# Optimization experiments

Hardware: AMD Instinct MI355X
Metric: run time of the kernel (lower is better)

## Reference

```python
import jax, jax.numpy as jnp
import numpy as np
import math

B, L, D, H, DFF = 8, 2048, 512, 8, 2048
FACTOR = 5

def setup_inputs() -> dict:
    key = jax.random.key(0)
    ks = jax.random.split(key, 20)
    r = lambda k, shape, s=0.02: (jax.random.normal(k, shape, jnp.float32) * s)
    return {
        'encoder_output': jax.random.normal(ks[0], (B, L, D), jnp.float32),
        'Wq': r(ks[1], (D, D)), 'bq': jnp.zeros((D,), jnp.float32),
        'Wk': r(ks[2], (D, D)), 'bk': jnp.zeros((D,), jnp.float32),
        'Wv': r(ks[3], (D, D)), 'bv': jnp.zeros((D,), jnp.float32),
        'Wo': r(ks[4], (D, D)), 'bo': jnp.zeros((D,), jnp.float32),
        'W1': r(ks[5], (DFF, D)), 'b1': jnp.zeros((DFF,), jnp.float32),
        'W2': r(ks[6], (D, DFF)), 'b2': jnp.zeros((D,), jnp.float32),
        'g1': jnp.ones((D,), jnp.float32), 'be1': jnp.zeros((D,), jnp.float32),
        'g2': jnp.ones((D,), jnp.float32), 'be2': jnp.zeros((D,), jnp.float32),
        'Wout': r(ks[7], (D, 1)), 'bout': jnp.zeros((1,), jnp.float32),
    }

def _layernorm(x, g, b, eps=1e-5):
    m = x.mean(-1, keepdims=True)
    v = x.var(-1, keepdims=True)
    return (x - m) / jnp.sqrt(v + eps) * g + b

def reference(encoder_output, Wq, bq, Wk, bk, Wv, bv, Wo, bo,
              W1, b1, W2, b2, g1, be1, g2, be2, Wout, bout):
    x = encoder_output  # [B, L, D]
    dh = D // H
    u = min(L, FACTOR * math.ceil(math.log(L)))  # number of active queries (static)

    # multi-head projections -> [B, H, L, dh]
    q = (x @ Wq + bq).reshape(B, L, H, dh).transpose(0, 2, 1, 3)
    k = (x @ Wk + bk).reshape(B, L, H, dh).transpose(0, 2, 1, 3)
    v = (x @ Wv + bv).reshape(B, L, H, dh).transpose(0, 2, 1, 3)

    # deterministic prob-sparse: sparsity measurement over all keys
    scores = jnp.einsum('bhld,bhsd->bhls', q, k) / math.sqrt(dh)  # [B,H,L,L]
    M = scores.max(-1) - scores.mean(-1)                           # [B,H,L]
    top_idx = jax.lax.top_k(M, u)[1]                               # [B,H,u]

    top_scores = jnp.take_along_axis(scores, top_idx[..., None], axis=2)  # [B,H,u,L]
    attn = jax.nn.softmax(top_scores, axis=-1)
    top_out = jnp.einsum('bhus,bhsd->bhud', attn, v)               # [B,H,u,dh]

    # lazy queries get mean(V); active queries get true attention
    ctx = jnp.broadcast_to(v.mean(axis=2, keepdims=True), (B, H, L, dh))
    bi = jnp.arange(B)[:, None, None]
    hi = jnp.arange(H)[None, :, None]
    ctx = ctx.at[bi, hi, top_idx].set(top_out)                     # [B,H,L,dh]

    attn_out = ctx.transpose(0, 2, 1, 3).reshape(B, L, D) @ Wo + bo  # [B,L,D]

    # decoder body: mean-pool, residual norms, pointwise conv FFN (eval-mode dropout = identity)
    a = attn_out.mean(axis=1)                 # [B, D]
    a = _layernorm(a + a, g1, be1)[:, None, :]  # [B, 1, D]  (a + dropout(a))

    ff = jax.nn.relu(a @ W1.T + b1)           # conv1d k=1 == linear, [B,1,DFF]
    ff = ff @ W2.T + b2                       # [B,1,D]
    out = _layernorm(a + ff, g2, be2)         # [B,1,D]

    forecasts = (out @ Wout + bout).squeeze(-1)  # [B,1]
    return forecasts, out
```

## Files before the change

### kernel.cpp

```cpp
#include <hip/hip_runtime.h>
#include <hip/hip_bf16.h>


#define B_   8
#define L_   2048
#define D_   512
#define H_   8
#define DH_  64
#define DFF_ 2048
#define U_   40
#define BH_  64
#define NM_  16384
#define NCK_ 16
#define CKS_ 128

typedef __bf16 bf16_t;
typedef __bf16 bf16x8 __attribute__((ext_vector_type(8)));
typedef float  f32x4  __attribute__((ext_vector_type(4)));

__device__ __forceinline__ void gl_lds16(const bf16_t* g, bf16_t* l) {
    __builtin_amdgcn_global_load_lds(
        (const __attribute__((address_space(1))) unsigned int*)g,
        (__attribute__((address_space(3))) unsigned int*)l, 16, 0, 0);
}

__global__ void k_cvt(const float* __restrict__ X, bf16_t* __restrict__ Xb) {
    size_t g = (size_t)blockIdx.x * 256 + threadIdx.x;
    const float4* xp = (const float4*)&X[g * 8];
    float4 f0 = xp[0], f1 = xp[1];
    bf16x8 hv;
    hv[0]=(bf16_t)f0.x; hv[1]=(bf16_t)f0.y; hv[2]=(bf16_t)f0.z; hv[3]=(bf16_t)f0.w;
    hv[4]=(bf16_t)f1.x; hv[5]=(bf16_t)f1.y; hv[6]=(bf16_t)f1.z; hv[7]=(bf16_t)f1.w;
    *(bf16x8*)&Xb[g * 8] = hv;
}

__global__ void k_transpose_w(const float* __restrict__ Wq, const float* __restrict__ Wk,
                              const float* __restrict__ Wv, bf16_t* __restrict__ WT) {
    __shared__ float tile[64][65];
    int blk = blockIdx.x;
    int mat = blk >> 6, tl = blk & 63;
    int tr = (tl >> 3) << 6;
    int tc = (tl & 7) << 6;
    const float* W = (mat == 0) ? Wq : (mat == 1) ? Wk : Wv;
    int t = threadIdx.x;
    #pragma unroll
    for (int i = 0; i < 16; ++i) {
        int e = t + i * 256, r = e >> 6, c = e & 63;
        tile[r][c] = W[(size_t)(tr + r) * 512 + tc + c];
    }
    __syncthreads();
    #pragma unroll
    for (int i = 0; i < 16; ++i) {
        int e = t + i * 256, r = e >> 6, c = e & 63;
        WT[(size_t)(mat * 512 + tc + r) * 512 + tr + c] = (bf16_t)tile[c][r];
    }
}

__global__ __launch_bounds__(256) void k_qkv(const bf16_t* __restrict__ Xb,
        const bf16_t* __restrict__ WT,
        const float* __restrict__ bq, const float* __restrict__ bk, const float* __restrict__ bv,
        bf16_t* __restrict__ Qb, bf16_t* __restrict__ Kb, float* __restrict__ Vf) {
    __shared__ bf16_t As[128 * 64];
    __shared__ bf16_t Bs[128 * 64];
    int t = threadIdx.x;
    int m0 = blockIdx.y * 128;
    int n0 = blockIdx.x * 128;
    int wv = t >> 6, lane = t & 63, lr = lane & 15, qd = lane >> 4;
    int wm = (wv & 1) * 64, wn = (wv >> 1) * 64;
    f32x4 acc[4][4];
    #pragma unroll
    for (int a = 0; a < 4; ++a)
        #pragma unroll
        for (int b = 0; b < 4; ++b) acc[a][b] = (f32x4){0.f, 0.f, 0.f, 0.f};

    for (int kt = 0; kt < 8; ++kt) {
        bf16x8 areg[4], breg[4];
        #pragma unroll
        for (int i = 0; i < 4; ++i) {
            int ch = i * 256 + t, r = ch >> 3, cs = ch & 7;
            areg[i] = *(const bf16x8*)&Xb[(size_t)(m0 + r) * 512 + kt * 64 + cs * 8];
            breg[i] = *(const bf16x8*)&WT[(size_t)(n0 + r) * 512 + kt * 64 + cs * 8];
        }
        __syncthreads();
        #pragma unroll
        for (int i = 0; i < 4; ++i) {
            int ch = i * 256 + t, r = ch >> 3, cs = ch & 7, c = cs ^ (r & 7);
            *(bf16x8*)&As[(r * 8 + c) * 8] = areg[i];
            *(bf16x8*)&Bs[(r * 8 + c) * 8] = breg[i];
        }
        __syncthreads();
        bf16x8 af[4][2], bfg[4][2];
        #pragma unroll
        for (int rf = 0; rf < 4; ++rf) {
            int row = wm + rf * 16 + lr;
            #pragma unroll
            for (int ks = 0; ks < 2; ++ks)
                af[rf][ks] = *(bf16x8*)&As[row * 64 + (((ks * 4 + qd) ^ (row & 7)) * 8)];
        }
        #pragma unroll
        for (int cf = 0; cf < 4; ++cf) {
            int row = wn + cf * 16 + lr;
            #pragma unroll
            for (int ks = 0; ks < 2; ++ks)
                bfg[cf][ks] = *(bf16x8*)&Bs[row * 64 + (((ks * 4 + qd) ^ (row & 7)) * 8)];
        }
        #pragma unroll
        for (int cf = 0; cf < 4; ++cf)
            #pragma unroll
            for (int rf = 0; rf < 4; ++rf) {
                acc[rf][cf] = __builtin_amdgcn_mfma_f32_16x16x32_bf16(af[rf][0], bfg[cf][0], acc[rf][cf], 0, 0, 0);
                acc[rf][cf] = __builtin_amdgcn_mfma_f32_16x16x32_bf16(af[rf][1], bfg[cf][1], acc[rf][cf], 0, 0, 0);
            }
    }
    int sec = n0 >> 9;
    const float* bias = (sec == 0) ? bq : (sec == 1) ? bk : bv;
    #pragma unroll
    for (int rf = 0; rf < 4; ++rf) {
        #pragma unroll
        for (int r = 0; r < 4; ++r) {
            int m = m0 + wm + rf * 16 + qd * 4 + r;
            int b = m >> 11, l = m & 2047;
            #pragma unroll
            for (int cf = 0; cf < 4; ++cf) {
                int n = n0 + wn + cf * 16 + lr;
                int nn = n & 511;
                int h = nn >> 6, d = nn & 63;
                float val = acc[rf][cf][r] + bias[nn];
                size_t oidx = ((size_t)(b * 8 + h) * L_ + l) * 64 + d;
                if (sec == 0)      Qb[oidx] = (bf16_t)val;
                else if (sec == 1) Kb[oidx] = (bf16_t)val;
                else               Vf[oidx] = val;
            }
        }
    }
}

__global__ __launch_bounds__(256) void k_rowmax(const bf16_t* __restrict__ Qb,
        const bf16_t* __restrict__ Kb, const float* __restrict__ kpart,
        float* __restrict__ Mv) {
    __shared__ bf16_t Ks[128 * 64];
    __shared__ float ksum_s[64];
    __shared__ float dot_s[128];
    int t = threadIdx.x;
    int bh = blockIdx.y;
    int row0 = blockIdx.x * 128;
    int wv = t >> 6, lane = t & 63, lr = lane & 15, qd = lane >> 4;
    size_t base = (size_t)bh * L_ * DH_;
    if (t < 64) {
        float a = 0.f;
        #pragma unroll
        for (int seg = 0; seg < 8; ++seg) a += kpart[(bh * 8 + seg) * 64 + t];
        ksum_s[t] = a;
    }
    bf16x8 af[2][2];
    #pragma unroll
    for (int rf = 0; rf < 2; ++rf)
        #pragma unroll
        for (int ks = 0; ks < 2; ++ks)
            af[rf][ks] = *(const bf16x8*)&Qb[base + (size_t)(row0 + wv * 32 + rf * 16 + lr) * 64 + ks * 32 + qd * 8];
    __syncthreads();
    #pragma unroll
    for (int rf = 0; rf < 2; ++rf) {
        float v = 0.f;
        #pragma unroll
        for (int ks = 0; ks < 2; ++ks)
            #pragma unroll
            for (int j = 0; j < 8; ++j)
                v += (float)af[rf][ks][j] * ksum_s[ks * 32 + qd * 8 + j];
        v += __shfl_xor(v, 16);
        v += __shfl_xor(v, 32);
        if (qd == 0) dot_s[wv * 32 + rf * 16 + lr] = v;
    }
    float pmax[2][4];
    #pragma unroll
    for (int a = 0; a < 2; ++a)
        #pragma unroll
        for (int r = 0; r < 4; ++r) pmax[a][r] = -3.4e38f;

    for (int cb = 0; cb < 16; ++cb) {
        bf16x8 kreg[4];
        #pragma unroll
        for (int i = 0; i < 4; ++i) {
            int ch = i * 256 + t, r = ch >> 3, cs = ch & 7;
            kreg[i] = *(const bf16x8*)&Kb[base + (size_t)(cb * 128 + r) * 64 + cs * 8];
        }
        __syncthreads();
        #pragma unroll
        for (int i = 0; i < 4; ++i) {
            int ch = i * 256 + t, r = ch >> 3, cs = ch & 7, c = cs ^ (r & 7);
            *(bf16x8*)&Ks[(r * 8 + c) * 8] = kreg[i];
        }
        __syncthreads();
        #pragma unroll
        for (int cf = 0; cf < 8; cf += 2) {
            int keyA = cf * 16 + lr, keyB = (cf + 1) * 16 + lr;
            bf16x8 bA0 = *(bf16x8*)&Ks[keyA * 64 + ((qd ^ (keyA & 7)) * 8)];
            bf16x8 bA1 = *(bf16x8*)&Ks[keyA * 64 + (((4 + qd) ^ (keyA & 7)) * 8)];
            bf16x8 bB0 = *(bf16x8*)&Ks[keyB * 64 + ((qd ^ (keyB & 7)) * 8)];
            bf16x8 bB1 = *(bf16x8*)&Ks[keyB * 64 + (((4 + qd) ^ (keyB & 7)) * 8)];
            #pragma unroll
            for (int rf = 0; rf < 2; ++rf) {
                f32x4 z = {0.f, 0.f, 0.f, 0.f};
                f32x4 c0 = __builtin_amdgcn_mfma_f32_16x16x32_bf16(af[rf][0], bA0, z, 0, 0, 0);
                c0 = __builtin_amdgcn_mfma_f32_16x16x32_bf16(af[rf][1], bA1, c0, 0, 0, 0);
                f32x4 c1 = __builtin_amdgcn_mfma_f32_16x16x32_bf16(af[rf][0], bB0, z, 0, 0, 0);
                c1 = __builtin_amdgcn_mfma_f32_16x16x32_bf16(af[rf][1], bB1, c1, 0, 0, 0);
                #pragma unroll
                for (int r = 0; r < 4; ++r)
                    pmax[rf][r] = fmaxf(pmax[rf][r], fmaxf(c0[r], c1[r]));
            }
        }
    }
    #pragma unroll
    for (int rf = 0; rf < 2; ++rf)
        #pragma unroll
        for (int r = 0; r < 4; ++r) {
            float v = pmax[rf][r];
            v = fmaxf(v, __shfl_xor(v, 1));
            v = fmaxf(v, __shfl_xor(v, 2));
            v = fmaxf(v, __shfl_xor(v, 4));
            v = fmaxf(v, __shfl_xor(v, 8));
            if (lr == 0) {
                int row = wv * 32 + rf * 16 + qd * 4 + r;
                Mv[bh * L_ + row0 + row] = v - dot_s[row] * (1.0f / 2048.0f);
            }
        }
}

__global__ void k_sums(const bf16_t* __restrict__ Kb, const float* __restrict__ Vf,
                       float* __restrict__ kpart, float* __restrict__ vpart) {
    __shared__ float red[32][64];
    int t = threadIdx.x;
    int seg = blockIdx.x, bh = blockIdx.y;
    int d8 = t & 7, g = t >> 3;
    size_t base = (size_t)bh * L_ * DH_ + (size_t)seg * 256 * DH_;
    float s[8];
    #pragma unroll
    for (int j = 0; j < 8; ++j) s[j] = 0.f;
    #pragma unroll
    for (int ss = 0; ss < 8; ++ss) {
        bf16x8 kk = *(const bf16x8*)&Kb[base + (size_t)(g * 8 + ss) * 64 + d8 * 8];
        #pragma unroll
        for (int j = 0; j < 8; ++j) s[j] += (float)kk[j];
    }
    #pragma unroll
    for (int j = 0; j < 8; ++j) red[g][d8 * 8 + j] = s[j];
    __syncthreads();
    if (t < 64) {
        float a = 0.f;
        #pragma unroll
        for (int gg = 0; gg < 32; ++gg) a += red[gg][t];
        kpart[(bh * 8 + seg) * 64 + t] = a;
    }
    __syncthreads();
    #pragma unroll
    for (int j = 0; j < 8; ++j) s[j] = 0.f;
    #pragma unroll
    for (int ss = 0; ss < 8; ++ss) {
        const float4* vp = (const float4*)&Vf[base + (size_t)(g * 8 + ss) * 64 + d8 * 8];
        float4 v0 = vp[0], v1 = vp[1];
        s[0]+=v0.x; s[1]+=v0.y; s[2]+=v0.z; s[3]+=v0.w;
        s[4]+=v1.x; s[5]+=v1.y; s[6]+=v1.z; s[7]+=v1.w;
    }
    __syncthreads();
    #pragma unroll
    for (int j = 0; j < 8; ++j) red[g][d8 * 8 + j] = s[j];
    __syncthreads();
    if (t < 64) {
        float a = 0.f;
        #pragma unroll
        for (int gg = 0; gg < 32; ++gg) a += red[gg][t];
        vpart[(bh * 8 + seg) * 64 + t] = a;
    }
}

__global__ void k_topk(const float* __restrict__ Mv, int* __restrict__ topidx) {
    int lane = threadIdx.x;
    int bh = blockIdx.x;
    unsigned key[32];
    #pragma unroll
    for (int j = 0; j < 32; ++j) {
        unsigned b = __float_as_uint(Mv[bh * L_ + j * 64 + lane]);
        key[j] = (b & 0x80000000u) ? ~b : (b | 0x80000000u);
    }
    unsigned lo = 0u, hi = 0xFFFFFFFFu;
    while (lo < hi) {
        unsigned mid = lo + ((hi - lo) >> 1) + 1;
        int c = 0;
        #pragma unroll
        for (int j = 0; j < 32; ++j)
            c += __popcll(__ballot(key[j] >= mid));
        if (c >= U_) lo = mid; else hi = mid - 1;
    }
    unsigned K40 = lo;
    int c_gt = 0;
    #pragma unroll
    for (int j = 0; j < 32; ++j)
        c_gt += __popcll(__ballot(key[j] > K40));
    unsigned long long lmask = (1ull << lane) - 1ull;
    int base_gt = 0, base_eq = 0;
    #pragma unroll
    for (int j = 0; j < 32; ++j) {
        bool gt = key[j] > K40, eq = key[j] == K40;
        unsigned long long mg = __ballot(gt);
        unsigned long long me = __ballot(eq);
        if (gt) {
            int pos = base_gt + __popcll(mg & lmask);
            topidx[bh * U_ + pos] = j * 64 + lane;
        } else if (eq) {
            int ep = base_eq + __popcll(me & lmask);
            if (c_gt + ep < U_)
                topidx[bh * U_ + c_gt + ep] = j * 64 + lane;
        }
        base_gt += __popcll(mg);
        base_eq += __popcll(me);
    }
}

__global__ __launch_bounds__(256) void k_attn2(const bf16_t* __restrict__ Qb,
        const bf16_t* __restrict__ Kb, const float* __restrict__ Vf,
        const int* __restrict__ topidx, float* __restrict__ part) {
    __shared__ bf16_t Qs[48 * 72];
    __shared__ bf16_t Ks[128 * 64];
    __shared__ bf16_t Vt[64 * 136];
    __shared__ float  wred[4][48];
    __shared__ float  frow[48];
    __shared__ int    tid_s[40];
    bf16_t* Ps = Ks;

    int t = threadIdx.x;
    int ck = blockIdx.x, bh = blockIdx.y;
    int c0 = ck * CKS_;
    size_t base = (size_t)bh * L_ * DH_;
    if (t < 40) tid_s[t] = topidx[bh * U_ + t];
    __syncthreads();
    #pragma unroll
    for (int i = 0; i < 4; ++i) {
        int s = i * 256 + t, r = s >> 3, cs = s & 7, c = cs ^ (r & 7);
        gl_lds16(&Kb[base + (size_t)(c0 + r) * 64 + c * 8], &Ks[s * 8]);
    }
    for (int e = t; e < 48 * 8; e += 256) {
        int r = e >> 3, c8 = e & 7;
        bf16x8 v;
        #pragma unroll
        for (int j = 0; j < 8; ++j) v[j] = (bf16_t)0.f;
        if (r < 40) v = *(const bf16x8*)&Qb[base + (size_t)tid_s[r] * 64 + c8 * 8];
        *(bf16x8*)&Qs[r * 72 + c8 * 8] = v;
    }
    #pragma unroll
    for (int i = 0; i < 8; ++i) {
        int e = t + i * 256;
        int key = e >> 4, d4 = e & 15;
        float4 v = *(const float4*)&Vf[base + (size_t)(c0 + key) * 64 + d4 * 4];
        Vt[(d4 * 4 + 0) * 136 + key] = (bf16_t)v.x;
        Vt[(d4 * 4 + 1) * 136 + key] = (bf16_t)v.y;
        Vt[(d4 * 4 + 2) * 136 + key] = (bf16_t)v.z;
        Vt[(d4 * 4 + 3) * 136 + key] = (bf16_t)v.w;
    }
    __syncthreads();

    int wv = t >> 6, lane = t & 63, lr = lane & 15, qd = lane >> 4;
    bf16x8 aq[3][2];
    #pragma unroll
    for (int tm = 0; tm < 3; ++tm)
        #pragma unroll
        for (int ks = 0; ks < 2; ++ks)
            aq[tm][ks] = *(bf16x8*)&Qs[(tm * 16 + lr) * 72 + ks * 32 + qd * 8];
    f32x4 S[3][2];
    #pragma unroll
    for (int nt = 0; nt < 2; ++nt) {
        int key = wv * 32 + nt * 16 + lr;
        bf16x8 bk0 = *(bf16x8*)&Ks[key * 64 + ((qd ^ (key & 7)) * 8)];
        bf16x8 bk1 = *(bf16x8*)&Ks[key * 64 + (((4 + qd) ^ (key & 7)) * 8)];
        #pragma unroll
        for (int tm = 0; tm < 3; ++tm) {
            f32x4 z = {0.f, 0.f, 0.f, 0.f};
            z = __builtin_amdgcn_mfma_f32_16x16x32_bf16(aq[tm][0], bk0, z, 0, 0, 0);
            S[tm][nt] = __builtin_amdgcn_mfma_f32_16x16x32_bf16(aq[tm][1], bk1, z, 0, 0, 0);
        }
    }
    float rm[3][4];
    #pragma unroll
    for (int tm = 0; tm < 3; ++tm)
        #pragma unroll
        for (int r = 0; r < 4; ++r) {
            float v = fmaxf(S[tm][0][r], S[tm][1][r]);
            v = fmaxf(v, __shfl_xor(v, 1));
            v = fmaxf(v, __shfl_xor(v, 2));
            v = fmaxf(v, __shfl_xor(v, 4));
            v = fmaxf(v, __shfl_xor(v, 8));
            rm[tm][r] = v;
        }
    if (lr == 0) {
        #pragma unroll
        for (int tm = 0; tm < 3; ++tm)
            #pragma unroll
            for (int r = 0; r < 4; ++r)
                wred[wv][tm * 16 + qd * 4 + r] = rm[tm][r];
    }
    __syncthreads();
    if (t < 48)
        frow[t] = fmaxf(fmaxf(wred[0][t], wred[1][t]), fmaxf(wred[2][t], wred[3][t]));
    __syncthreads();
    float rs_[3][4];
    #pragma unroll
    for (int tm = 0; tm < 3; ++tm) {
        #pragma unroll
        for (int r = 0; r < 4; ++r) {
            float fm = frow[tm * 16 + qd * 4 + r];
            float s0 = __expf((S[tm][0][r] - fm) * 0.125f);
            float s1 = __expf((S[tm][1][r] - fm) * 0.125f);
            Ps[(tm * 16 + qd * 4 + r) * 136 + wv * 32 + lr]      = (bf16_t)s0;
            Ps[(tm * 16 + qd * 4 + r) * 136 + wv * 32 + 16 + lr] = (bf16_t)s1;
            rs_[tm][r] = s0 + s1;
        }
    }
    #pragma unroll
    for (int tm = 0; tm < 3; ++tm)
        #pragma unroll
        for (int r = 0; r < 4; ++r) {
            float v = rs_[tm][r];
            v += __shfl_xor(v, 1);
            v += __shfl_xor(v, 2);
            v += __shfl_xor(v, 4);
            v += __shfl_xor(v, 8);
            rs_[tm][r] = v;
        }
    if (lr == 0) {
        #pragma unroll
        for (int tm = 0; tm < 3; ++tm)
            #pragma unroll
            for (int r = 0; r < 4; ++r)
                wred[wv][tm * 16 + qd * 4 + r] = rs_[tm][r];
    }
    __syncthreads();
    float* pb = &part[(((size_t)bh * NCK_ + ck) * 40) * 66];
    if (t < 40) {
        pb[t * 66 + 64] = frow[t] * 0.125f;
        pb[t * 66 + 65] = wred[0][t] + wred[1][t] + wred[2][t] + wred[3][t];
    }
    f32x4 O[3];
    #pragma unroll
    for (int tm = 0; tm < 3; ++tm) O[tm] = (f32x4){0.f, 0.f, 0.f, 0.f};
    #pragma unroll
    for (int kk = 0; kk < 4; ++kk) {
        bf16x8 bv = *(bf16x8*)&Vt[(wv * 16 + lr) * 136 + kk * 32 + qd * 8];
        #pragma unroll
        for (int tm = 0; tm < 3; ++tm) {
            bf16x8 ap = *(bf16x8*)&Ps[(tm * 16 + lr) * 136 + kk * 32 + qd * 8];
            O[tm] = __builtin_amdgcn_mfma_f32_16x16x32_bf16(ap, bv, O[tm], 0, 0, 0);
        }
    }
    #pragma unroll
    for (int tm = 0; tm < 3; ++tm)
        #pragma unroll
        for (int r = 0; r < 4; ++r) {
            int row = tm * 16 + qd * 4 + r;
            if (row < 40) pb[row * 66 + wv * 16 + lr] = O[tm][r];
        }
}

__global__ void k_attnred(const float* __restrict__ part, float* __restrict__ tout) {
    int t = threadIdx.x, bh = blockIdx.x;
    int d = t & 63, rg = t >> 6;
    const float* pb0 = &part[((size_t)bh * NCK_) * 40 * 66];
    for (int ri = 0; ri < 10; ++ri) {
        int r = rg + 4 * ri;
        float M = -3.4e38f;
        #pragma unroll
        for (int c = 0; c < NCK_; ++c) M = fmaxf(M, pb0[(c * 40 + r) * 66 + 64]);
        float lsum = 0.f, osum = 0.f;
        #pragma unroll
        for (int c = 0; c < NCK_; ++c) {
            float w = __expf(pb0[(c * 40 + r) * 66 + 64] - M);
            lsum += w * pb0[(c * 40 + r) * 66 + 65];
            osum += w * pb0[(c * 40 + r) * 66 + d];
        }
        tout[((size_t)bh * U_ + r) * 64 + d] = osum / lsum;
    }
}

__global__ void k_ctx(const float* __restrict__ vpart, const float* __restrict__ topout,
                      const float* __restrict__ Wo, const float* __restrict__ bo,
                      const float* __restrict__ g1, const float* __restrict__ be1,
                      float* __restrict__ a2) {
    __shared__ float cm[512];
    __shared__ float rs[256], rq[256];
    int t = threadIdx.x, b = blockIdx.x;
    #pragma unroll
    for (int p = 0; p < 2; ++p) {
        int hd = t + p * 256;
        int h = hd >> 6, dd = hd & 63;
        int bh = b * 8 + h;
        float vs = 0.f;
        #pragma unroll
        for (int seg = 0; seg < 8; ++seg) vs += vpart[(bh * 8 + seg) * 64 + dd];
        float tsum = 0.f;
        for (int ii = 0; ii < U_; ++ii) tsum += topout[((size_t)bh * U_ + ii) * 64 + dd];
        cm[hd] = (0.98046875f * vs + tsum) * (1.0f / 2048.0f);
    }
    __syncthreads();
    float x[2];
    #pragma unroll
    for (int p = 0; p < 2; ++p) {
        int j = t + p * 256;
        float acc = bo[j];
        for (int c = 0; c < 128; ++c) {
            float4 cv = *(const float4*)&cm[c * 4];
            acc += cv.x * Wo[(size_t)(c * 4 + 0) * 512 + j];
            acc += cv.y * Wo[(size_t)(c * 4 + 1) * 512 + j];
            acc += cv.z * Wo[(size_t)(c * 4 + 2) * 512 + j];
            acc += cv.w * Wo[(size_t)(c * 4 + 3) * 512 + j];
        }
        x[p] = 2.0f * acc;
    }
    rs[t] = x[0] + x[1];
    rq[t] = x[0] * x[0] + x[1] * x[1];
    __syncthreads();
    for (int str = 128; str > 0; str >>= 1) {
        if (t < str) { rs[t] += rs[t + str]; rq[t] += rq[t + str]; }
        __syncthreads();
    }
    float mean = rs[0] * (1.0f / 512.0f);
    float var  = rq[0] * (1.0f / 512.0f) - mean * mean;
    float rstd = rsqrtf(var + 1e-5f);
    #pragma unroll
    for (int p = 0; p < 2; ++p) {
        int j = t + p * 256;
        a2[b * 512 + j] = (x[p] - mean) * rstd * g1[j] + be1[j];
    }
}

__global__ void k_ff1p(const float* __restrict__ a2, const float* __restrict__ W1,
                       float* __restrict__ ffp) {
    __shared__ float Ws[64 * 132];
    __shared__ float as[8 * 128];
    int t = threadIdx.x;
    int jb = blockIdx.x, seg = blockIdx.y;
    int j0 = jb * 64, c0 = seg * 128;
    #pragma unroll
    for (int i = 0; i < 8; ++i) {
        int e = t + i * 256;
        int r = e >> 5, c4 = e & 31;
        *(float4*)&Ws[r * 132 + c4 * 4] =
            *(const float4*)&W1[(size_t)(j0 + r) * 512 + c0 + c4 * 4];
    }
    for (int e = t; e < 1024; e += 256) {
        int b = e >> 7, c = e & 127;
        as[b * 128 + c] = a2[b * 512 + c0 + c];
    }
    __syncthreads();
    int j = t & 63, bp = t >> 6;
    float acc0 = 0.f, acc1 = 0.f;
    for (int c = 0; c < 32; ++c) {
        float4 w  = *(float4*)&Ws[j * 132 + c * 4];
        float4 xa = *(float4*)&as[(bp * 2) * 128 + c * 4];
        float4 xb = *(float4*)&as[(bp * 2 + 1) * 128 + c * 4];
        acc0 += w.x * xa.x + w.y * xa.y + w.z * xa.z + w.w * xa.w;
        acc1 += w.x * xb.x + w.y * xb.y + w.z * xb.z + w.w * xb.w;
    }
    ffp[(size_t)(seg * 8 + bp * 2) * 2048 + j0 + j]     = acc0;
    ffp[(size_t)(seg * 8 + bp * 2 + 1) * 2048 + j0 + j] = acc1;
}

__global__ void k_ffr(const float* __restrict__ ffp, const float* __restrict__ b1v,
                      float* __restrict__ ffb) {
    int e = blockIdx.x * 256 + threadIdx.x;
    int b = e >> 11, j = e & 2047;
    float s = b1v[j];
    #pragma unroll
    for (int seg = 0; seg < 4; ++seg) s += ffp[(size_t)(seg * 8 + b) * 2048 + j];
    ffb[b * 2048 + j] = fmaxf(s, 0.f);
}

__global__ void k_ff2p(const float* __restrict__ ffb, const float* __restrict__ W2,
                       float* __restrict__ ff2p) {
    __shared__ float Ws[32 * 260];
    __shared__ float fs[8 * 256];
    int t = threadIdx.x;
    int db = blockIdx.x, seg = blockIdx.y;
    int d0 = db * 32, c0 = seg * 256;
    #pragma unroll
    for (int i = 0; i < 8; ++i) {
        int e = t + i * 256;
        int r = e >> 6, c4 = e & 63;
        *(float4*)&Ws[r * 260 + c4 * 4] =
            *(const float4*)&W2[(size_t)(d0 + r) * 2048 + c0 + c4 * 4];
    }
    for (int e = t; e < 2048; e += 256) {
        int b = e >> 8, c = e & 255;
        fs[b * 256 + c] = ffb[b * 2048 + c0 + c];
    }
    __syncthreads();
    int d = t & 31, b = t >> 5;
    float acc = 0.f;
    for (int c = 0; c < 64; ++c) {
        float4 w = *(float4*)&Ws[d * 260 + c * 4];
        float4 x = *(float4*)&fs[b * 256 + c * 4];
        acc += w.x * x.x + w.y * x.y + w.z * x.z + w.w * x.w;
    }
    ff2p[(size_t)(seg * 8 + b) * 512 + d0 + d] = acc;
}

__global__ void k_final(const float* __restrict__ a2, const float* __restrict__ ff2p,
                        const float* __restrict__ b2v,
                        const float* __restrict__ g2, const float* __restrict__ be2,
                        const float* __restrict__ Wout, const float* __restrict__ bout,
                        float* __restrict__ dout) {
    __shared__ float rs[256], rq[256];
    int t = threadIdx.x, b = blockIdx.x;
    float f0 = b2v[t], f1 = b2v[t + 256];
    #pragma unroll
    for (int seg = 0; seg < 8; ++seg) {
        f0 += ff2p[(size_t)(seg * 8 + b) * 512 + t];
        f1 += ff2p[(size_t)(seg * 8 + b) * 512 + t + 256];
    }
    float x0 = a2[b * 512 + t] + f0;
    float x1 = a2[b * 512 + t + 256] + f1;
    rs[t] = x0 + x1;
    rq[t] = x0 * x0 + x1 * x1;
    __syncthreads();
    for (int str = 128; str > 0; str >>= 1) {
        if (t < str) { rs[t] += rs[t + str]; rq[t] += rq[t + str]; }
        __syncthreads();
    }
    float mean = rs[0] * (1.0f / 512.0f);
    float var  = rq[0] * (1.0f / 512.0f) - mean * mean;
    float rstd = rsqrtf(var + 1e-5f);
    float o0 = (x0 - mean) * rstd * g2[t]       + be2[t];
    float o1 = (x1 - mean) * rstd * g2[t + 256] + be2[t + 256];
    dout[8 + b * 512 + t]       = o0;
    dout[8 + b * 512 + t + 256] = o1;
    __syncthreads();
    rs[t] = o0 * Wout[t] + o1 * Wout[t + 256];
    __syncthreads();
    for (int str = 128; str > 0; str >>= 1) {
        if (t < str) rs[t] += rs[t + str];
        __syncthreads();
    }
    if (t == 0) dout[b] = rs[0] + bout[0];
}

extern "C" void kernel_launch(void* const* d_in, const int* in_sizes, int n_in,
                              void* d_out, int out_size, void* d_ws, size_t ws_size,
                              hipStream_t stream) {
    const float* X    = (const float*)d_in[0];
    const float* Wq   = (const float*)d_in[1];
    const float* bq   = (const float*)d_in[2];
    const float* Wk   = (const float*)d_in[3];
    const float* bk   = (const float*)d_in[4];
    const float* Wv   = (const float*)d_in[5];
    const float* bv   = (const float*)d_in[6];
    const float* Wo   = (const float*)d_in[7];
    const float* bo   = (const float*)d_in[8];
    const float* W1   = (const float*)d_in[9];
    const float* b1   = (const float*)d_in[10];
    const float* W2   = (const float*)d_in[11];
    const float* b2   = (const float*)d_in[12];
    const float* g1   = (const float*)d_in[13];
    const float* be1  = (const float*)d_in[14];
    const float* g2   = (const float*)d_in[15];
    const float* be2  = (const float*)d_in[16];
    const float* Wout = (const float*)d_in[17];
    const float* bout = (const float*)d_in[18];
    float* out = (float*)d_out;

    char* ws = (char*)d_ws;
    size_t off = 0;
    auto alloc = [&](size_t bytes) -> void* {
        void* p = ws + off;
        off += (bytes + 255) & ~(size_t)255;
        return p;
    };
    bf16_t* Xb   = (bf16_t*)alloc((size_t)NM_ * D_ * 2);
    bf16_t* WT   = (bf16_t*)alloc((size_t)1536 * 512 * 2);
    bf16_t* Qb   = (bf16_t*)alloc((size_t)BH_ * L_ * DH_ * 2);
    bf16_t* Kb   = (bf16_t*)alloc((size_t)BH_ * L_ * DH_ * 2);
    float*  Vf   = (float*) alloc((size_t)BH_ * L_ * DH_ * 4);
    float*  Mv   = (float*) alloc((size_t)BH_ * L_ * 4);
    float*  kpart= (float*) alloc((size_t)BH_ * 8 * 64 * 4);
    float*  vpart= (float*) alloc((size_t)BH_ * 8 * 64 * 4);
    int*    tidx = (int*)   alloc((size_t)BH_ * U_ * 4);
    float*  tout = (float*) alloc((size_t)BH_ * U_ * 64 * 4);
    float*  a2   = (float*) alloc(8 * 512 * 4);
    float*  ffp  = (float*) alloc((size_t)4 * 8 * 2048 * 4);
    float*  ffb  = (float*) alloc(8 * 2048 * 4);
    float*  ff2p = (float*) alloc((size_t)8 * 8 * 512 * 4);
    float*  part = (float*)Xb;
    (void)ws_size; (void)in_sizes; (void)n_in; (void)out_size;

    hipLaunchKernelGGL(k_cvt,         dim3(4096),       dim3(256), 0, stream, X, Xb);
    hipLaunchKernelGGL(k_transpose_w, dim3(192),        dim3(256), 0, stream, Wq, Wk, Wv, WT);
    hipLaunchKernelGGL(k_qkv,         dim3(12, 128),    dim3(256), 0, stream, Xb, WT, bq, bk, bv, Qb, Kb, Vf);
    hipLaunchKernelGGL(k_sums,        dim3(8, 64),      dim3(256), 0, stream, Kb, Vf, kpart, vpart);
    hipLaunchKernelGGL(k_rowmax,      dim3(16, 64),     dim3(256), 0, stream, Qb, Kb, kpart, Mv);
    hipLaunchKernelGGL(k_topk,        dim3(64),         dim3(64),  0, stream, Mv, tidx);
    hipLaunchKernelGGL(k_attn2,       dim3(NCK_, 64),   dim3(256), 0, stream, Qb, Kb, Vf, tidx, part);
    hipLaunchKernelGGL(k_attnred,     dim3(64),         dim3(256), 0, stream, part, tout);
    hipLaunchKernelGGL(k_ctx,         dim3(8),          dim3(256), 0, stream, vpart, tout, Wo, bo, g1, be1, a2);
    hipLaunchKernelGGL(k_ff1p,        dim3(32, 4),      dim3(256), 0, stream, a2, W1, ffp);
    hipLaunchKernelGGL(k_ffr,         dim3(64),         dim3(256), 0, stream, ffp, b1, ffb);
    hipLaunchKernelGGL(k_ff2p,        dim3(16, 8),      dim3(256), 0, stream, ffb, W2, ff2p);
    hipLaunchKernelGGL(k_final,       dim3(8),          dim3(256), 0, stream, a2, ff2p, b2, g2, be2, Wout, bout, out);
}
```

Before: 311.8 us.

## Fuse K/V column sums into QKV GEMM, store V as bf16, merge small kernels

The K and V column sums are now computed in the QKV GEMM epilogue through an LDS reduction, which removes the separate k_sums pass that reread K and V. V is stored as bf16 instead of fp32, halving its write and read traffic in attention. The input convert and weight transpose are merged into one launch, and the FFN bias+ReLU reduction is folded into k_ff2p, cutting launch count. V precision drops to bf16, and the sums now use more partial segments.

```diff
diff --git a/kernel.cpp b/kernel.cpp
--- a/kernel.cpp
+++ b/kernel.cpp
@@ -18,31 +18,26 @@
 typedef __bf16 bf16x8 __attribute__((ext_vector_type(8)));
 typedef float  f32x4  __attribute__((ext_vector_type(4)));
 
-__device__ __forceinline__ void gl_lds16(const bf16_t* g, bf16_t* l) {
-    __builtin_amdgcn_global_load_lds(
-        (const __attribute__((address_space(1))) unsigned int*)g,
-        (__attribute__((address_space(3))) unsigned int*)l, 16, 0, 0);
-}
-
-__global__ void k_cvt(const float* __restrict__ X, bf16_t* __restrict__ Xb) {
-    size_t g = (size_t)blockIdx.x * 256 + threadIdx.x;
-    const float4* xp = (const float4*)&X[g * 8];
-    float4 f0 = xp[0], f1 = xp[1];
-    bf16x8 hv;
-    hv[0]=(bf16_t)f0.x; hv[1]=(bf16_t)f0.y; hv[2]=(bf16_t)f0.z; hv[3]=(bf16_t)f0.w;
-    hv[4]=(bf16_t)f1.x; hv[5]=(bf16_t)f1.y; hv[6]=(bf16_t)f1.z; hv[7]=(bf16_t)f1.w;
-    *(bf16x8*)&Xb[g * 8] = hv;
-}
-
-__global__ void k_transpose_w(const float* __restrict__ Wq, const float* __restrict__ Wk,
-                              const float* __restrict__ Wv, bf16_t* __restrict__ WT) {
+__global__ void k_prep(const float* __restrict__ X, bf16_t* __restrict__ Xb,
+                       const float* __restrict__ Wq, const float* __restrict__ Wk,
+                       const float* __restrict__ Wv, bf16_t* __restrict__ WT) {
     __shared__ float tile[64][65];
-    int blk = blockIdx.x;
+    int t = threadIdx.x;
+    if (blockIdx.x < 4096) {
+        size_t g = (size_t)blockIdx.x * 256 + t;
+        const float4* xp = (const float4*)&X[g * 8];
+        float4 f0 = xp[0], f1 = xp[1];
+        bf16x8 hv;
+        hv[0]=(bf16_t)f0.x; hv[1]=(bf16_t)f0.y; hv[2]=(bf16_t)f0.z; hv[3]=(bf16_t)f0.w;
+        hv[4]=(bf16_t)f1.x; hv[5]=(bf16_t)f1.y; hv[6]=(bf16_t)f1.z; hv[7]=(bf16_t)f1.w;
+        *(bf16x8*)&Xb[g * 8] = hv;
+        return;
+    }
+    int blk = blockIdx.x - 4096;
     int mat = blk >> 6, tl = blk & 63;
     int tr = (tl >> 3) << 6;
     int tc = (tl & 7) << 6;
     const float* W = (mat == 0) ? Wq : (mat == 1) ? Wk : Wv;
-    int t = threadIdx.x;
     #pragma unroll
     for (int i = 0; i < 16; ++i) {
         int e = t + i * 256, r = e >> 6, c = e & 63;
@@ -59,7 +54,8 @@
 __global__ __launch_bounds__(256) void k_qkv(const bf16_t* __restrict__ Xb,
         const bf16_t* __restrict__ WT,
         const float* __restrict__ bq, const float* __restrict__ bk, const float* __restrict__ bv,
-        bf16_t* __restrict__ Qb, bf16_t* __restrict__ Kb, float* __restrict__ Vf) {
+        bf16_t* __restrict__ Qb, bf16_t* __restrict__ Kb, bf16_t* __restrict__ Vb,
+        float* __restrict__ kpart, float* __restrict__ vpart) {
     __shared__ bf16_t As[128 * 64];
     __shared__ bf16_t Bs[128 * 64];
     int t = threadIdx.x;
@@ -114,6 +110,7 @@
     }
     int sec = n0 >> 9;
     const float* bias = (sec == 0) ? bq : (sec == 1) ? bk : bv;
+    float colsum[4] = {0.f, 0.f, 0.f, 0.f};
     #pragma unroll
     for (int rf = 0; rf < 4; ++rf) {
         #pragma unroll
@@ -126,11 +123,31 @@
                 int nn = n & 511;
                 int h = nn >> 6, d = nn & 63;
                 float val = acc[rf][cf][r] + bias[nn];
+                colsum[cf] += val;
                 size_t oidx = ((size_t)(b * 8 + h) * L_ + l) * 64 + d;
                 if (sec == 0)      Qb[oidx] = (bf16_t)val;
                 else if (sec == 1) Kb[oidx] = (bf16_t)val;
-                else               Vf[oidx] = val;
+                else               Vb[oidx] = (bf16_t)val;
             }
+        }
+    }
+    if (sec != 0) {
+        float* sred = (float*)As;
+        __syncthreads();
+        int g = (wv & 1) * 4 + qd;
+        #pragma unroll
+        for (int cf = 0; cf < 4; ++cf)
+            sred[(wn + cf * 16 + lr) * 8 + g] = colsum[cf];
+        __syncthreads();
+        if (t < 128) {
+            float s = 0.f;
+            #pragma unroll
+            for (int gg = 0; gg < 8; ++gg) s += sred[t * 8 + gg];
+            int nn = (n0 + t) & 511;
+            int h = nn >> 6, d = nn & 63;
+            int b = blockIdx.y >> 4, seg = blockIdx.y & 15;
+            float* dst = (sec == 1) ? kpart : vpart;
+            dst[(((size_t)(b * 8 + h)) * 16 + seg) * 64 + d] = s;
         }
     }
 }
@@ -149,7 +166,7 @@
     if (t < 64) {
         float a = 0.f;
         #pragma unroll
-        for (int seg = 0; seg < 8; ++seg) a += kpart[(bh * 8 + seg) * 64 + t];
+        for (int seg = 0; seg < 16; ++seg) a += kpart[((size_t)bh * 16 + seg) * 64 + t];
         ksum_s[t] = a;
     }
     bf16x8 af[2][2];
@@ -225,53 +242,6 @@
                 Mv[bh * L_ + row0 + row] = v - dot_s[row] * (1.0f / 2048.0f);
             }
         }
-}
-
-__global__ void k_sums(const bf16_t* __restrict__ Kb, const float* __restrict__ Vf,
-                       float* __restrict__ kpart, float* __restrict__ vpart) {
-    __shared__ float red[32][64];
-    int t = threadIdx.x;
-    int seg = blockIdx.x, bh = blockIdx.y;
-    int d8 = t & 7, g = t >> 3;
-    size_t base = (size_t)bh * L_ * DH_ + (size_t)seg * 256 * DH_;
-    float s[8];
-    #pragma unroll
-    for (int j = 0; j < 8; ++j) s[j] = 0.f;
-    #pragma unroll
-    for (int ss = 0; ss < 8; ++ss) {
-        bf16x8 kk = *(const bf16x8*)&Kb[base + (size_t)(g * 8 + ss) * 64 + d8 * 8];
-        #pragma unroll
-        for (int j = 0; j < 8; ++j) s[j] += (float)kk[j];
-    }
-    #pragma unroll
-    for (int j = 0; j < 8; ++j) red[g][d8 * 8 + j] = s[j];
-    __syncthreads();
-    if (t < 64) {
-        float a = 0.f;
-        #pragma unroll
-        for (int gg = 0; gg < 32; ++gg) a += red[gg][t];
-        kpart[(bh * 8 + seg) * 64 + t] = a;
-    }
-    __syncthreads();
-    #pragma unroll
-    for (int j = 0; j < 8; ++j) s[j] = 0.f;
-    #pragma unroll
-    for (int ss = 0; ss < 8; ++ss) {
-        const float4* vp = (const float4*)&Vf[base + (size_t)(g * 8 + ss) * 64 + d8 * 8];
-        float4 v0 = vp[0], v1 = vp[1];
-        s[0]+=v0.x; s[1]+=v0.y; s[2]+=v0.z; s[3]+=v0.w;
-        s[4]+=v1.x; s[5]+=v1.y; s[6]+=v1.z; s[7]+=v1.w;
-    }
-    __syncthreads();
-    #pragma unroll
-    for (int j = 0; j < 8; ++j) red[g][d8 * 8 + j] = s[j];
-    __syncthreads();
-    if (t < 64) {
-        float a = 0.f;
-        #pragma unroll
-        for (int gg = 0; gg < 32; ++gg) a += red[gg][t];
-        vpart[(bh * 8 + seg) * 64 + t] = a;
-    }
 }
 
 __global__ void k_topk(const float* __restrict__ Mv, int* __restrict__ topidx) {
@@ -318,7 +288,7 @@
 }
 
 __global__ __launch_bounds__(256) void k_attn2(const bf16_t* __restrict__ Qb,
-        const bf16_t* __restrict__ Kb, const float* __restrict__ Vf,
+        const bf16_t* __restrict__ Kb, const bf16_t* __restrict__ Vb,
         const int* __restrict__ topidx, float* __restrict__ part) {
     __shared__ bf16_t Qs[48 * 72];
     __shared__ bf16_t Ks[128 * 64];
@@ -333,12 +303,18 @@
     int c0 = ck * CKS_;
     size_t base = (size_t)bh * L_ * DH_;
     if (t < 40) tid_s[t] = topidx[bh * U_ + t];
-    __syncthreads();
+    bf16x8 kreg[4];
+    #pragma unroll
+    for (int i = 0; i < 4; ++i) {
+        int s = i * 256 + t, r = s >> 3, cs = s & 7;
+        kreg[i] = *(const bf16x8*)&Kb[base + (size_t)(c0 + r) * 64 + cs * 8];
+    }
     #pragma unroll
     for (int i = 0; i < 4; ++i) {
         int s = i * 256 + t, r = s >> 3, cs = s & 7, c = cs ^ (r & 7);
-        gl_lds16(&Kb[base + (size_t)(c0 + r) * 64 + c * 8], &Ks[s * 8]);
-    }
+        *(bf16x8*)&Ks[(r * 8 + c) * 8] = kreg[i];
+    }
+    __syncthreads();
     for (int e = t; e < 48 * 8; e += 256) {
         int r = e >> 3, c8 = e & 7;
         bf16x8 v;
@@ -348,14 +324,13 @@
         *(bf16x8*)&Qs[r * 72 + c8 * 8] = v;
     }
     #pragma unroll
-    for (int i = 0; i < 8; ++i) {
+    for (int i = 0; i < 4; ++i) {
         int e = t + i * 256;
-        int key = e >> 4, d4 = e & 15;
-        float4 v = *(const float4*)&Vf[base + (size_t)(c0 + key) * 64 + d4 * 4];
-        Vt[(d4 * 4 + 0) * 136 + key] = (bf16_t)v.x;
-        Vt[(d4 * 4 + 1) * 136 + key] = (bf16_t)v.y;
-        Vt[(d4 * 4 + 2) * 136 + key] = (bf16_t)v.z;
-        Vt[(d4 * 4 + 3) * 136 + key] = (bf16_t)v.w;
+        int key = e >> 3, c8 = e & 7;
+        bf16x8 v = *(const bf16x8*)&Vb[base + (size_t)(c0 + key) * 64 + c8 * 8];
+        #pragma unroll
+        for (int j = 0; j < 8; ++j)
+            Vt[(c8 * 8 + j) * 136 + key] = v[j];
     }
     __syncthreads();
 
@@ -494,7 +469,7 @@
         int bh = b * 8 + h;
         float vs = 0.f;
         #pragma unroll
-        for (int seg = 0; seg < 8; ++seg) vs += vpart[(bh * 8 + seg) * 64 + dd];
+        for (int seg = 0; seg < 16; ++seg) vs += vpart[((size_t)bh * 16 + seg) * 64 + dd];
         float tsum = 0.f;
         for (int ii = 0; ii < U_; ++ii) tsum += topout[((size_t)bh * U_ + ii) * 64 + dd];
         cm[hd] = (0.98046875f * vs + tsum) * (1.0f / 2048.0f);
@@ -563,18 +538,8 @@
     ffp[(size_t)(seg * 8 + bp * 2 + 1) * 2048 + j0 + j] = acc1;
 }
 
-__global__ void k_ffr(const float* __restrict__ ffp, const float* __restrict__ b1v,
-                      float* __restrict__ ffb) {
-    int e = blockIdx.x * 256 + threadIdx.x;
-    int b = e >> 11, j = e & 2047;
-    float s = b1v[j];
-    #pragma unroll
-    for (int seg = 0; seg < 4; ++seg) s += ffp[(size_t)(seg * 8 + b) * 2048 + j];
-    ffb[b * 2048 + j] = fmaxf(s, 0.f);
-}
-
-__global__ void k_ff2p(const float* __restrict__ ffb, const float* __restrict__ W2,
-                       float* __restrict__ ff2p) {
+__global__ void k_ff2p(const float* __restrict__ ffp, const float* __restrict__ b1v,
+                       const float* __restrict__ W2, float* __restrict__ ff2p) {
     __shared__ float Ws[32 * 260];
     __shared__ float fs[8 * 256];
     int t = threadIdx.x;
@@ -589,7 +554,10 @@
     }
     for (int e = t; e < 2048; e += 256) {
         int b = e >> 8, c = e & 255;
-        fs[b * 256 + c] = ffb[b * 2048 + c0 + c];
+        float s = b1v[c0 + c];
+        #pragma unroll
+        for (int sg = 0; sg < 4; ++sg) s += ffp[(size_t)(sg * 8 + b) * 2048 + c0 + c];
+        fs[b * 256 + c] = fmaxf(s, 0.f);
     }
     __syncthreads();
     int d = t & 31, b = t >> 5;
@@ -676,30 +644,26 @@
     bf16_t* WT   = (bf16_t*)alloc((size_t)1536 * 512 * 2);
     bf16_t* Qb   = (bf16_t*)alloc((size_t)BH_ * L_ * DH_ * 2);
     bf16_t* Kb   = (bf16_t*)alloc((size_t)BH_ * L_ * DH_ * 2);
-    float*  Vf   = (float*) alloc((size_t)BH_ * L_ * DH_ * 4);
+    bf16_t* Vb   = (bf16_t*)alloc((size_t)BH_ * L_ * DH_ * 2);
     float*  Mv   = (float*) alloc((size_t)BH_ * L_ * 4);
-    float*  kpart= (float*) alloc((size_t)BH_ * 8 * 64 * 4);
-    float*  vpart= (float*) alloc((size_t)BH_ * 8 * 64 * 4);
+    float*  kpart= (float*) alloc((size_t)BH_ * 16 * 64 * 4);
+    float*  vpart= (float*) alloc((size_t)BH_ * 16 * 64 * 4);
     int*    tidx = (int*)   alloc((size_t)BH_ * U_ * 4);
     float*  tout = (float*) alloc((size_t)BH_ * U_ * 64 * 4);
     float*  a2   = (float*) alloc(8 * 512 * 4);
     float*  ffp  = (float*) alloc((size_t)4 * 8 * 2048 * 4);
-    float*  ffb  = (float*) alloc(8 * 2048 * 4);
     float*  ff2p = (float*) alloc((size_t)8 * 8 * 512 * 4);
     float*  part = (float*)Xb;
     (void)ws_size; (void)in_sizes; (void)n_in; (void)out_size;
 
-    hipLaunchKernelGGL(k_cvt,         dim3(4096),       dim3(256), 0, stream, X, Xb);
-    hipLaunchKernelGGL(k_transpose_w, dim3(192),        dim3(256), 0, stream, Wq, Wk, Wv, WT);
-    hipLaunchKernelGGL(k_qkv,         dim3(12, 128),    dim3(256), 0, stream, Xb, WT, bq, bk, bv, Qb, Kb, Vf);
-    hipLaunchKernelGGL(k_sums,        dim3(8, 64),      dim3(256), 0, stream, Kb, Vf, kpart, vpart);
-    hipLaunchKernelGGL(k_rowmax,      dim3(16, 64),     dim3(256), 0, stream, Qb, Kb, kpart, Mv);
-    hipLaunchKernelGGL(k_topk,        dim3(64),         dim3(64),  0, stream, Mv, tidx);
-    hipLaunchKernelGGL(k_attn2,       dim3(NCK_, 64),   dim3(256), 0, stream, Qb, Kb, Vf, tidx, part);
-    hipLaunchKernelGGL(k_attnred,     dim3(64),         dim3(256), 0, stream, part, tout);
-    hipLaunchKernelGGL(k_ctx,         dim3(8),          dim3(256), 0, stream, vpart, tout, Wo, bo, g1, be1, a2);
-    hipLaunchKernelGGL(k_ff1p,        dim3(32, 4),      dim3(256), 0, stream, a2, W1, ffp);
-    hipLaunchKernelGGL(k_ffr,         dim3(64),         dim3(256), 0, stream, ffp, b1, ffb);
-    hipLaunchKernelGGL(k_ff2p,        dim3(16, 8),      dim3(256), 0, stream, ffb, W2, ff2p);
-    hipLaunchKernelGGL(k_final,       dim3(8),          dim3(256), 0, stream, a2, ff2p, b2, g2, be2, Wout, bout, out);
-}
+    hipLaunchKernelGGL(k_prep,    dim3(4096 + 192), dim3(256), 0, stream, X, Xb, Wq, Wk, Wv, WT);
+    hipLaunchKernelGGL(k_qkv,     dim3(12, 128),    dim3(256), 0, stream, Xb, WT, bq, bk, bv, Qb, Kb, Vb, kpart, vpart);
+    hipLaunchKernelGGL(k_rowmax,  dim3(16, 64),     dim3(256), 0, stream, Qb, Kb, kpart, Mv);
+    hipLaunchKernelGGL(k_topk,    dim3(64),         dim3(64),  0, stream, Mv, tidx);
+    hipLaunchKernelGGL(k_attn2,   dim3(NCK_, 64),   dim3(256), 0, stream, Qb, Kb, Vb, tidx, part);
+    hipLaunchKernelGGL(k_attnred, dim3(64),         dim3(256), 0, stream, part, tout);
+    hipLaunchKernelGGL(k_ctx,     dim3(8),          dim3(256), 0, stream, vpart, tout, Wo, bo, g1, be1, a2);
+    hipLaunchKernelGGL(k_ff1p,    dim3(32, 4),      dim3(256), 0, stream, a2, W1, ffp);
+    hipLaunchKernelGGL(k_ff2p,    dim3(16, 8),      dim3(256), 0, stream, ffp, b1, W2, ff2p);
+    hipLaunchKernelGGL(k_final,   dim3(8),          dim3(256), 0, stream, a2, ff2p, b2, g2, be2, Wout, bout, out);
+}
```

Measured after the change: 293.2 us. 6.0% less time.
